# Kernel optimization log

Measured on AMD Instinct MI355X. Metric: run time of the kernel, lower is better.

The kernel has to match this reference:

```python
import jax, jax.numpy as jnp
import numpy as np
import math

NUM_NODES = 100000
NUM_SCORES = 64

def mish(x):
    return x * jnp.tanh(jax.nn.softplus(x))

def setup_inputs() -> dict:
    key = jax.random.key(0)
    k1, k2, k3, k4 = jax.random.split(key, 4)
    N, F = 1000000, 256
    data = jax.random.normal(k1, (N, F), dtype=jnp.float32)
    tokens_to_node_map = jax.random.randint(k2, (N,), 0, NUM_NODES, dtype=jnp.int64)
    # ensure max index == NUM_NODES-1 so num_nodes matches torch's max()+1
    tokens_to_node_map = tokens_to_node_map.at[-1].set(NUM_NODES - 1)
    W = jax.random.normal(k3, (F, NUM_SCORES), dtype=jnp.float32) * math.sqrt(2.0 / (F + NUM_SCORES))
    b = jnp.zeros((NUM_SCORES,), dtype=jnp.float32)
    scoring = jax.random.normal(k4, (NUM_SCORES, 1), dtype=jnp.float32) * math.sqrt(2.0 / (NUM_SCORES + 1))
    return {"data": data, "tokens_to_node_map": tokens_to_node_map, "W": W, "b": b, "scoring": scoring}

def reference(data, tokens_to_node_map, W, b, scoring):
    # dead score chain, faithfully replicated from the original module
    s = data @ W + b                              # (N', num_scores)
    s = s @ scoring                               # (N', 1)
    s = s / math.sqrt(NUM_SCORES)
    s = mish(s)
    s = s - jnp.max(s)
    exp_s = jnp.exp(s)
    # original overwrites exp scores with ones -> segment-mean pooling
    exp_s = jnp.ones_like(exp_s)
    seg_sum = jax.ops.segment_sum(exp_s, tokens_to_node_map, num_segments=NUM_NODES)  # (num_nodes, 1)
    weights = exp_s / seg_sum[tokens_to_node_map]                                     # (N', 1)
    nodes_feature = jax.ops.segment_sum(data * weights, tokens_to_node_map, num_segments=NUM_NODES)
    return nodes_feature
```

## Files before the change

kernel.cpp:

```cpp
#include <hip/hip_runtime.h>

#define NN 100000
#define TILE 256
#define NB ((NN + TILE - 1) / TILE)

typedef float floatx4 __attribute__((ext_vector_type(4)));

__global__ void asl_count_kernel(const int* __restrict__ map,
                                 unsigned int* __restrict__ cnt, int n) {
    int i = blockIdx.x * blockDim.x + threadIdx.x;
    int stride = gridDim.x * blockDim.x;
    for (; i < n; i += stride) {
        atomicAdd(&cnt[map[i]], 1u);
    }
}

__global__ void asl_blocksum_kernel(const unsigned int* __restrict__ cnt,
                                    unsigned int* __restrict__ blocksum) {
    __shared__ unsigned int sh[TILE];
    int t = threadIdx.x, b = blockIdx.x;
    int i = b * TILE + t;
    unsigned int v = (i < NN) ? cnt[i] : 0u;
    sh[t] = v;
    __syncthreads();
    for (int off = TILE / 2; off > 0; off >>= 1) {
        if (t < off) sh[t] += sh[t + off];
        __syncthreads();
    }
    if (t == 0) blocksum[b] = sh[0];
}

__global__ __launch_bounds__(512)
void asl_scanblocks_kernel(const unsigned int* __restrict__ blocksum,
                           unsigned int* __restrict__ blockoff) {
    __shared__ unsigned int sh[512];
    int t = threadIdx.x;
    unsigned int v = (t < NB) ? blocksum[t] : 0u;
    sh[t] = v;
    __syncthreads();
    for (int off = 1; off < 512; off <<= 1) {
        unsigned int y = (t >= off) ? sh[t - off] : 0u;
        __syncthreads();
        sh[t] += y;
        __syncthreads();
    }
    if (t < NB) blockoff[t] = sh[t] - v;
}

__global__ void asl_scantiles_kernel(const unsigned int* __restrict__ cnt,
                                     const unsigned int* __restrict__ blockoff,
                                     unsigned int* __restrict__ base,
                                     unsigned int* __restrict__ next) {
    __shared__ unsigned int sh[TILE];
    int t = threadIdx.x, b = blockIdx.x;
    int i = b * TILE + t;
    unsigned int v = (i < NN) ? cnt[i] : 0u;
    sh[t] = v;
    __syncthreads();
    for (int off = 1; off < TILE; off <<= 1) {
        unsigned int y = (t >= off) ? sh[t - off] : 0u;
        __syncthreads();
        sh[t] += y;
        __syncthreads();
    }
    unsigned int excl = sh[t] - v + blockoff[b];
    if (i < NN) {
        base[i] = excl;
        next[i] = excl;
    }
}

__global__ void asl_fill_kernel(const int* __restrict__ map,
                                unsigned int* __restrict__ next,
                                int* __restrict__ list, int n) {
    int i = blockIdx.x * blockDim.x + threadIdx.x;
    int stride = gridDim.x * blockDim.x;
    for (; i < n; i += stride) {
        unsigned int pos = atomicAdd(&next[map[i]], 1u);
        list[pos] = i;
    }
}

__global__ void asl_gather_kernel(const floatx4* __restrict__ data,
                                  const int* __restrict__ list,
                                  const unsigned int* __restrict__ base,
                                  const unsigned int* __restrict__ cnt,
                                  floatx4* __restrict__ out, int num_nodes) {
    long long tid = (long long)blockIdx.x * blockDim.x + threadIdx.x;
    int node = (int)(tid >> 6);
    if (node >= num_nodes) return;
    int lane = (int)(tid & 63);

    unsigned int b = base[node];
    unsigned int c = cnt[node];

    floatx4 a0 = {0.f, 0.f, 0.f, 0.f};
    floatx4 a1 = {0.f, 0.f, 0.f, 0.f};

    for (unsigned int j0 = 0; j0 < c; j0 += 64) {
        unsigned int rem = min(64u, c - j0);
        int tl = (lane < (int)rem) ? list[b + j0 + lane] : 0;

        unsigned int j = 0;
        for (; j + 4 <= rem; j += 4) {
            int t0 = __shfl(tl, (int)j);
            int t1 = __shfl(tl, (int)j + 1);
            int t2 = __shfl(tl, (int)j + 2);
            int t3 = __shfl(tl, (int)j + 3);
            floatx4 v0 = __builtin_nontemporal_load(&data[(size_t)t0 * 64 + lane]);
            floatx4 v1 = __builtin_nontemporal_load(&data[(size_t)t1 * 64 + lane]);
            floatx4 v2 = __builtin_nontemporal_load(&data[(size_t)t2 * 64 + lane]);
            floatx4 v3 = __builtin_nontemporal_load(&data[(size_t)t3 * 64 + lane]);
            a0 += v0; a1 += v1; a0 += v2; a1 += v3;
        }
        for (; j < rem; ++j) {
            int t0 = __shfl(tl, (int)j);
            a0 += __builtin_nontemporal_load(&data[(size_t)t0 * 64 + lane]);
        }
    }

    float w = c ? (1.0f / (float)c) : 0.0f;
    floatx4 r = (a0 + a1) * w;
    __builtin_nontemporal_store(r, &out[(size_t)node * 64 + lane]);
}

extern "C" void kernel_launch(void* const* d_in, const int* in_sizes, int n_in,
                              void* d_out, int out_size, void* d_ws, size_t ws_size,
                              hipStream_t stream) {
    const float* data = (const float*)d_in[0];
    const int*   map  = (const int*)d_in[1];

    const int n_tokens = in_sizes[1];
    float* out = (float*)d_out;

    unsigned int* ws       = (unsigned int*)d_ws;
    unsigned int* cnt      = ws;
    unsigned int* base     = ws + NN;
    unsigned int* next     = ws + 2 * NN;
    int*          list     = (int*)(ws + 3 * NN);
    unsigned int* blocksum = ws + 3 * NN + n_tokens;
    unsigned int* blockoff = ws + 3 * NN + n_tokens + NB;

    hipMemsetAsync(cnt, 0, (size_t)NN * sizeof(unsigned int), stream);

    {
        int block = 256;
        int grid = (n_tokens + block - 1) / block;
        asl_count_kernel<<<grid, block, 0, stream>>>(map, cnt, n_tokens);
    }
    asl_blocksum_kernel<<<NB, TILE, 0, stream>>>(cnt, blocksum);
    asl_scanblocks_kernel<<<1, 512, 0, stream>>>(blocksum, blockoff);
    asl_scantiles_kernel<<<NB, TILE, 0, stream>>>(cnt, blockoff, base, next);
    {
        int block = 256;
        int grid = (n_tokens + block - 1) / block;
        asl_fill_kernel<<<grid, block, 0, stream>>>(map, next, list, n_tokens);
    }
    {
        int block = 256;
        long long total = (long long)NN * 64;
        int grid = (int)((total + block - 1) / block);
        asl_gather_kernel<<<grid, block, 0, stream>>>(
            (const floatx4*)data, list, base, cnt, (floatx4*)out, NN);
    }
}
```

Measured before the change: 344.1 us.

## Merge scan kernels, vectorize map reads, and deepen gather unroll

Merges the block-offset scan into the tile-scan kernel, with every block redundantly scanning the block sums, which drops one launch. Tiles grow to 512. The count and fill kernels now read the map as int4 vectors. The gather derives each node's count from adjacent base entries instead of reading cnt, unrolls to 8 loads with 4 accumulators, and loads list entries with nontemporal hints. The aim is fewer launches and more memory-level parallelism in the bandwidth-bound gather, at the cost of redundant scan work per block and higher register pressure.

```diff
diff --git a/kernel.cpp b/kernel.cpp
--- a/kernel.cpp
+++ b/kernel.cpp
@@ -1,90 +1,106 @@
 #include <hip/hip_runtime.h>
 
 #define NN 100000
-#define TILE 256
-#define NB ((NN + TILE - 1) / TILE)
+#define STILE 512
+#define SNB ((NN + STILE - 1) / STILE)
 
 typedef float floatx4 __attribute__((ext_vector_type(4)));
-
-__global__ void asl_count_kernel(const int* __restrict__ map,
+typedef int   intx4   __attribute__((ext_vector_type(4)));
+
+__global__ void asl_count_kernel(const intx4* __restrict__ map4,
+                                 const int* __restrict__ map,
                                  unsigned int* __restrict__ cnt, int n) {
+    int n4 = n >> 2;
     int i = blockIdx.x * blockDim.x + threadIdx.x;
     int stride = gridDim.x * blockDim.x;
-    for (; i < n; i += stride) {
-        atomicAdd(&cnt[map[i]], 1u);
-    }
-}
-
-__global__ void asl_blocksum_kernel(const unsigned int* __restrict__ cnt,
-                                    unsigned int* __restrict__ blocksum) {
-    __shared__ unsigned int sh[TILE];
+    for (; i < n4; i += stride) {
+        intx4 m = map4[i];
+        atomicAdd(&cnt[m.x], 1u);
+        atomicAdd(&cnt[m.y], 1u);
+        atomicAdd(&cnt[m.z], 1u);
+        atomicAdd(&cnt[m.w], 1u);
+    }
+    if (blockIdx.x == 0 && threadIdx.x < (n & 3)) {
+        atomicAdd(&cnt[map[(n4 << 2) + threadIdx.x]], 1u);
+    }
+}
+
+__global__ __launch_bounds__(STILE)
+void asl_blocksum_kernel(const unsigned int* __restrict__ cnt,
+                         unsigned int* __restrict__ blocksum) {
+    __shared__ unsigned int sh[STILE];
     int t = threadIdx.x, b = blockIdx.x;
-    int i = b * TILE + t;
+    int i = b * STILE + t;
+    sh[t] = (i < NN) ? cnt[i] : 0u;
+    __syncthreads();
+    for (int off = STILE / 2; off > 0; off >>= 1) {
+        if (t < off) sh[t] += sh[t + off];
+        __syncthreads();
+    }
+    if (t == 0) blocksum[b] = sh[0];
+}
+
+__global__ __launch_bounds__(STILE)
+void asl_scantiles_kernel(const unsigned int* __restrict__ cnt,
+                          const unsigned int* __restrict__ blocksum,
+                          unsigned int* __restrict__ base,
+                          unsigned int* __restrict__ next) {
+    __shared__ unsigned int sh[STILE];
+    int t = threadIdx.x, b = blockIdx.x;
+
+    sh[t] = (t < SNB) ? blocksum[t] : 0u;
+    __syncthreads();
+    for (int off = 1; off < STILE; off <<= 1) {
+        unsigned int y = (t >= off) ? sh[t - off] : 0u;
+        __syncthreads();
+        sh[t] += y;
+        __syncthreads();
+    }
+    unsigned int blockoff = (b == 0) ? 0u : sh[b - 1];
+    __syncthreads();
+
+    int i = b * STILE + t;
     unsigned int v = (i < NN) ? cnt[i] : 0u;
     sh[t] = v;
     __syncthreads();
-    for (int off = TILE / 2; off > 0; off >>= 1) {
-        if (t < off) sh[t] += sh[t + off];
-        __syncthreads();
-    }
-    if (t == 0) blocksum[b] = sh[0];
-}
-
-__global__ __launch_bounds__(512)
-void asl_scanblocks_kernel(const unsigned int* __restrict__ blocksum,
-                           unsigned int* __restrict__ blockoff) {
-    __shared__ unsigned int sh[512];
-    int t = threadIdx.x;
-    unsigned int v = (t < NB) ? blocksum[t] : 0u;
-    sh[t] = v;
-    __syncthreads();
-    for (int off = 1; off < 512; off <<= 1) {
+    for (int off = 1; off < STILE; off <<= 1) {
         unsigned int y = (t >= off) ? sh[t - off] : 0u;
         __syncthreads();
         sh[t] += y;
         __syncthreads();
     }
-    if (t < NB) blockoff[t] = sh[t] - v;
-}
-
-__global__ void asl_scantiles_kernel(const unsigned int* __restrict__ cnt,
-                                     const unsigned int* __restrict__ blockoff,
-                                     unsigned int* __restrict__ base,
-                                     unsigned int* __restrict__ next) {
-    __shared__ unsigned int sh[TILE];
-    int t = threadIdx.x, b = blockIdx.x;
-    int i = b * TILE + t;
-    unsigned int v = (i < NN) ? cnt[i] : 0u;
-    sh[t] = v;
-    __syncthreads();
-    for (int off = 1; off < TILE; off <<= 1) {
-        unsigned int y = (t >= off) ? sh[t - off] : 0u;
-        __syncthreads();
-        sh[t] += y;
-        __syncthreads();
-    }
-    unsigned int excl = sh[t] - v + blockoff[b];
+    unsigned int excl = blockoff + sh[t] - v;
     if (i < NN) {
         base[i] = excl;
         next[i] = excl;
-    }
-}
-
-__global__ void asl_fill_kernel(const int* __restrict__ map,
+        if (i == NN - 1) base[NN] = excl + v;
+    }
+}
+
+__global__ void asl_fill_kernel(const intx4* __restrict__ map4,
+                                const int* __restrict__ map,
                                 unsigned int* __restrict__ next,
                                 int* __restrict__ list, int n) {
+    int n4 = n >> 2;
     int i = blockIdx.x * blockDim.x + threadIdx.x;
     int stride = gridDim.x * blockDim.x;
-    for (; i < n; i += stride) {
-        unsigned int pos = atomicAdd(&next[map[i]], 1u);
-        list[pos] = i;
+    for (; i < n4; i += stride) {
+        intx4 m = map4[i];
+        int tok = i << 2;
+        list[atomicAdd(&next[m.x], 1u)] = tok;
+        list[atomicAdd(&next[m.y], 1u)] = tok + 1;
+        list[atomicAdd(&next[m.z], 1u)] = tok + 2;
+        list[atomicAdd(&next[m.w], 1u)] = tok + 3;
+    }
+    if (blockIdx.x == 0 && threadIdx.x < (n & 3)) {
+        int tok = (n4 << 2) + threadIdx.x;
+        list[atomicAdd(&next[map[tok]], 1u)] = tok;
     }
 }
 
 __global__ void asl_gather_kernel(const floatx4* __restrict__ data,
                                   const int* __restrict__ list,
                                   const unsigned int* __restrict__ base,
-                                  const unsigned int* __restrict__ cnt,
                                   floatx4* __restrict__ out, int num_nodes) {
     long long tid = (long long)blockIdx.x * blockDim.x + threadIdx.x;
     int node = (int)(tid >> 6);
@@ -92,26 +108,45 @@
     int lane = (int)(tid & 63);
 
     unsigned int b = base[node];
-    unsigned int c = cnt[node];
-
-    floatx4 a0 = {0.f, 0.f, 0.f, 0.f};
-    floatx4 a1 = {0.f, 0.f, 0.f, 0.f};
+    unsigned int c = base[node + 1] - b;
+
+    floatx4 a0 = {0.f,0.f,0.f,0.f}, a1 = {0.f,0.f,0.f,0.f};
+    floatx4 a2 = {0.f,0.f,0.f,0.f}, a3 = {0.f,0.f,0.f,0.f};
 
     for (unsigned int j0 = 0; j0 < c; j0 += 64) {
         unsigned int rem = min(64u, c - j0);
-        int tl = (lane < (int)rem) ? list[b + j0 + lane] : 0;
+        int tl = (lane < (int)rem) ? __builtin_nontemporal_load(&list[b + j0 + lane]) : 0;
 
         unsigned int j = 0;
+        for (; j + 8 <= rem; j += 8) {
+            int t0 = __shfl(tl, (int)j);
+            int t1 = __shfl(tl, (int)j + 1);
+            int t2 = __shfl(tl, (int)j + 2);
+            int t3 = __shfl(tl, (int)j + 3);
+            int t4 = __shfl(tl, (int)j + 4);
+            int t5 = __shfl(tl, (int)j + 5);
+            int t6 = __shfl(tl, (int)j + 6);
+            int t7 = __shfl(tl, (int)j + 7);
+            floatx4 v0 = __builtin_nontemporal_load(&data[(size_t)t0 * 64 + lane]);
+            floatx4 v1 = __builtin_nontemporal_load(&data[(size_t)t1 * 64 + lane]);
+            floatx4 v2 = __builtin_nontemporal_load(&data[(size_t)t2 * 64 + lane]);
+            floatx4 v3 = __builtin_nontemporal_load(&data[(size_t)t3 * 64 + lane]);
+            floatx4 v4 = __builtin_nontemporal_load(&data[(size_t)t4 * 64 + lane]);
+            floatx4 v5 = __builtin_nontemporal_load(&data[(size_t)t5 * 64 + lane]);
+            floatx4 v6 = __builtin_nontemporal_load(&data[(size_t)t6 * 64 + lane]);
+            floatx4 v7 = __builtin_nontemporal_load(&data[(size_t)t7 * 64 + lane]);
+            a0 += v0; a1 += v1; a2 += v2; a3 += v3;
+            a0 += v4; a1 += v5; a2 += v6; a3 += v7;
+        }
         for (; j + 4 <= rem; j += 4) {
             int t0 = __shfl(tl, (int)j);
             int t1 = __shfl(tl, (int)j + 1);
             int t2 = __shfl(tl, (int)j + 2);
             int t3 = __shfl(tl, (int)j + 3);
-            floatx4 v0 = __builtin_nontemporal_load(&data[(size_t)t0 * 64 + lane]);
-            floatx4 v1 = __builtin_nontemporal_load(&data[(size_t)t1 * 64 + lane]);
-            floatx4 v2 = __builtin_nontemporal_load(&data[(size_t)t2 * 64 + lane]);
-            floatx4 v3 = __builtin_nontemporal_load(&data[(size_t)t3 * 64 + lane]);
-            a0 += v0; a1 += v1; a0 += v2; a1 += v3;
+            a0 += __builtin_nontemporal_load(&data[(size_t)t0 * 64 + lane]);
+            a1 += __builtin_nontemporal_load(&data[(size_t)t1 * 64 + lane]);
+            a2 += __builtin_nontemporal_load(&data[(size_t)t2 * 64 + lane]);
+            a3 += __builtin_nontemporal_load(&data[(size_t)t3 * 64 + lane]);
         }
         for (; j < rem; ++j) {
             int t0 = __shfl(tl, (int)j);
@@ -120,7 +155,7 @@
     }
 
     float w = c ? (1.0f / (float)c) : 0.0f;
-    floatx4 r = (a0 + a1) * w;
+    floatx4 r = ((a0 + a1) + (a2 + a3)) * w;
     __builtin_nontemporal_store(r, &out[(size_t)node * 64 + lane]);
 }
 
@@ -136,31 +171,31 @@
     unsigned int* ws       = (unsigned int*)d_ws;
     unsigned int* cnt      = ws;
     unsigned int* base     = ws + NN;
-    unsigned int* next     = ws + 2 * NN;
-    int*          list     = (int*)(ws + 3 * NN);
-    unsigned int* blocksum = ws + 3 * NN + n_tokens;
-    unsigned int* blockoff = ws + 3 * NN + n_tokens + NB;
+    unsigned int* next     = ws + 2 * NN + 1;
+    int*          list     = (int*)(ws + 3 * NN + 1);
+    unsigned int* blocksum = ws + 3 * NN + 1 + n_tokens;
 
     hipMemsetAsync(cnt, 0, (size_t)NN * sizeof(unsigned int), stream);
 
     {
         int block = 256;
-        int grid = (n_tokens + block - 1) / block;
-        asl_count_kernel<<<grid, block, 0, stream>>>(map, cnt, n_tokens);
-    }
-    asl_blocksum_kernel<<<NB, TILE, 0, stream>>>(cnt, blocksum);
-    asl_scanblocks_kernel<<<1, 512, 0, stream>>>(blocksum, blockoff);
-    asl_scantiles_kernel<<<NB, TILE, 0, stream>>>(cnt, blockoff, base, next);
+        int grid = ((n_tokens >> 2) + block - 1) / block;
+        asl_count_kernel<<<grid, block, 0, stream>>>(
+            (const intx4*)map, map, cnt, n_tokens);
+    }
+    asl_blocksum_kernel<<<SNB, STILE, 0, stream>>>(cnt, blocksum);
+    asl_scantiles_kernel<<<SNB, STILE, 0, stream>>>(cnt, blocksum, base, next);
     {
         int block = 256;
-        int grid = (n_tokens + block - 1) / block;
-        asl_fill_kernel<<<grid, block, 0, stream>>>(map, next, list, n_tokens);
+        int grid = ((n_tokens >> 2) + block - 1) / block;
+        asl_fill_kernel<<<grid, block, 0, stream>>>(
+            (const intx4*)map, map, next, list, n_tokens);
     }
     {
         int block = 256;
         long long total = (long long)NN * 64;
         int grid = (int)((total + block - 1) / block);
         asl_gather_kernel<<<grid, block, 0, stream>>>(
-            (const floatx4*)data, list, base, cnt, (floatx4*)out, NN);
-    }
-}
+            (const floatx4*)data, list, base, (floatx4*)out, NN);
+    }
+}
```

Result: faster. 326.2 us (-5.2%).
